# Performance work log

Hardware: AMD Instinct MI355X
Metric: run time of the kernel (lower is better)

Reference implementation:

```python
import jax, jax.numpy as jnp
import numpy as np

S = 4096      # total packed tokens
B = 8         # number of variable-length segments
E = 1152      # embed_dim (SigLIP2 so400m)
H = 16        # num_heads
D = E // H    # head_dim = 72


def setup_inputs() -> dict:
    key = jax.random.key(0)
    ks = jax.random.split(key, 8)
    w_std = 0.02
    theta = jax.random.uniform(ks[1], (S, D), jnp.float32, 0.0, 2.0 * np.pi)
    return {
        "hidden_states": jax.random.normal(ks[0], (S, E), jnp.float32),
        "cu_seqlens": jnp.arange(B + 1, dtype=jnp.int32) * (S // B),
        "cos": jnp.cos(theta),
        "sin": jnp.sin(theta),
        "Wq": jax.random.normal(ks[2], (E, E), jnp.float32) * w_std,
        "bq": jnp.zeros((E,), jnp.float32),
        "Wk": jax.random.normal(ks[3], (E, E), jnp.float32) * w_std,
        "bk": jnp.zeros((E,), jnp.float32),
        "Wv": jax.random.normal(ks[4], (E, E), jnp.float32) * w_std,
        "bv": jnp.zeros((E,), jnp.float32),
        "Wo": jax.random.normal(ks[5], (E, E), jnp.float32) * w_std,
        "bo": jnp.zeros((E,), jnp.float32),
    }


def _rotate_half(x):
    x1, x2 = jnp.split(x, 2, axis=-1)
    return jnp.concatenate((-x2, x1), axis=-1)


def reference(hidden_states, cu_seqlens, cos, sin, Wq, bq, Wk, bk, Wv, bv, Wo, bo):
    seq_len = hidden_states.shape[0]
    scale = np.float32(D) ** -0.5
    # projections -> [S, H, D]
    q = (hidden_states @ Wq.T + bq).reshape(seq_len, H, D)
    k = (hidden_states @ Wk.T + bk).reshape(seq_len, H, D)
    v = (hidden_states @ Wv.T + bv).reshape(seq_len, H, D)
    # inline RoPE (apply_rotary_pos_emb_vision): cos/sin broadcast over heads
    c = cos[:, None, :]
    s = sin[:, None, :]
    q = q * c + _rotate_half(q) * s
    k = k * c + _rotate_half(k) * s
    # segment id per token from cu_seqlens; block-diagonal attention mask
    seg = jnp.searchsorted(cu_seqlens[1:], jnp.arange(seq_len, dtype=cu_seqlens.dtype), side="right")
    mask = seg[:, None] == seg[None, :]                     # [S, S]
    scores = jnp.einsum("shd,thd->hst", q, k) * scale       # [H, S, S]
    neg = jnp.finfo(scores.dtype).min
    scores = jnp.where(mask[None, :, :], scores, neg)
    probs = jax.nn.softmax(scores, axis=-1)
    attn = jnp.einsum("hst,thd->shd", probs, v).reshape(seq_len, E)
    return attn @ Wo.T + bo
```

## Files before the change

kernel.cpp:

```cpp
#include <hip/hip_runtime.h>
#include <float.h>

#define S_LEN 4096
#define E_DIM 1152
#define NH    16
#define HD    72
#define HD2   36
#define NQKV  3456

typedef __attribute__((ext_vector_type(4))) float f32x4;
typedef __attribute__((ext_vector_type(8))) _Float16 f16x8;

__device__ __forceinline__ unsigned short f2h(float f) {
    union { _Float16 h; unsigned short u; } c;
    c.h = (_Float16)f;
    return c.u;
}

__device__ __forceinline__ void gload_lds16(const unsigned short* g, unsigned short* l) {
    __builtin_amdgcn_global_load_lds(
        (const __attribute__((address_space(1))) unsigned int*)g,
        (__attribute__((address_space(3))) unsigned int*)l, 16, 0, 0);
}

__global__ __launch_bounds__(256)
void pack_f16(const float* __restrict__ hs, const float* __restrict__ wq,
              const float* __restrict__ wk, const float* __restrict__ wv,
              const float* __restrict__ wo,
              unsigned short* __restrict__ hs_h, unsigned short* __restrict__ wqkv_h,
              unsigned short* __restrict__ wo_h)
{
    const float* src; unsigned short* dst; int n4;
    const int WSZ = E_DIM * E_DIM;
    switch (blockIdx.z) {
        case 0: src = hs; dst = hs_h;             n4 = S_LEN * E_DIM / 4; break;
        case 1: src = wq; dst = wqkv_h;           n4 = WSZ / 4; break;
        case 2: src = wk; dst = wqkv_h + WSZ;     n4 = WSZ / 4; break;
        case 3: src = wv; dst = wqkv_h + 2 * WSZ; n4 = WSZ / 4; break;
        default: src = wo; dst = wo_h;            n4 = WSZ / 4; break;
    }
    for (int i = blockIdx.x * 256 + threadIdx.x; i < n4; i += gridDim.x * 256) {
        f32x4 x = ((const f32x4*)src)[i];
        ushort4 hv;
        hv.x = f2h(x[0]); hv.y = f2h(x[1]); hv.z = f2h(x[2]); hv.w = f2h(x[3]);
        ((ushort4*)dst)[i] = hv;
    }
}

__global__ __launch_bounds__(256, 4)
void gemm_qkv_f16(const unsigned short* __restrict__ Ah, const unsigned short* __restrict__ Wh,
                  const float* __restrict__ bq, const float* __restrict__ bk,
                  const float* __restrict__ bv,
                  float* __restrict__ oq, float* __restrict__ ok,
                  unsigned short* __restrict__ vt)
{
    __shared__ unsigned short sA[128 * 64];
    __shared__ unsigned short sB[128 * 64];
    const int tid  = threadIdx.x;
    const int w    = tid >> 6, lane = tid & 63;
    const int quad = lane >> 4, m = lane & 15;
    const int wr   = w & 1,  wc = w >> 1;

    const int bid = blockIdx.x;
    const int lin = (bid & 7) * 108 + (bid >> 3);
    const int n_t = lin >> 5;
    const int m_t = lin & 31;
    const int m0  = m_t * 128;
    const int n0  = n_t * 128;

    const int srow = lane >> 3;
    const int skc  = (lane & 7) ^ srow;

    f32x4 acc[4][4];
    #pragma unroll
    for (int i = 0; i < 4; ++i)
        #pragma unroll
        for (int j = 0; j < 4; ++j) acc[i][j] = (f32x4){0.f, 0.f, 0.f, 0.f};

    const int rm7 = m & 7;

    for (int k0 = 0; k0 < E_DIM; k0 += 64) {
        #pragma unroll
        for (int c = 0; c < 4; ++c) {
            int r = 32 * w + 8 * c + srow;
            gload_lds16(Ah + (size_t)(m0 + r) * E_DIM + k0 + skc * 8, &sA[(32 * w + 8 * c) * 64]);
            gload_lds16(Wh + (size_t)(n0 + r) * E_DIM + k0 + skc * 8, &sB[(32 * w + 8 * c) * 64]);
        }
        __syncthreads();

        #pragma unroll
        for (int k3 = 0; k3 < 2; ++k3) {
            f16x8 ah[4], bh[4];
            #pragma unroll
            for (int t = 0; t < 4; ++t) {
                int pc = ((k3 << 2) + quad) ^ rm7;
                ah[t] = *(const f16x8*)&sA[(64 * wr + 16 * t + m) * 64 + pc * 8];
                bh[t] = *(const f16x8*)&sB[(64 * wc + 16 * t + m) * 64 + pc * 8];
            }
            #pragma unroll
            for (int rt = 0; rt < 4; ++rt)
                #pragma unroll
                for (int ct = 0; ct < 4; ++ct)
                    acc[rt][ct] = __builtin_amdgcn_mfma_f32_16x16x32_f16(ah[rt], bh[ct], acc[rt][ct], 0, 0, 0);
        }
        __syncthreads();
    }

    const int which = n0 / E_DIM;
    const int n0l = n0 - which * E_DIM;
    if (which < 2) {
        const float* bp = (which == 0) ? bq : bk;
        float* Cp       = (which == 0) ? oq : ok;
        #pragma unroll
        for (int ct = 0; ct < 4; ++ct) {
            int col = n0l + 64 * wc + 16 * ct + m;
            float bias = bp[col];
            #pragma unroll
            for (int rt = 0; rt < 4; ++rt)
                #pragma unroll
                for (int reg = 0; reg < 4; ++reg) {
                    int row = m0 + 64 * wr + 16 * rt + 4 * quad + reg;
                    Cp[(size_t)row * E_DIM + col] = acc[rt][ct][reg] + bias;
                }
        }
    } else {
        #pragma unroll
        for (int ct = 0; ct < 4; ++ct) {
            int vcol = n0l + 64 * wc + 16 * ct + m;
            int hh = vcol / HD, dd = vcol - hh * HD;
            float bias = bv[vcol];
            unsigned short* vrow = vt + ((size_t)hh * HD + dd) * S_LEN;
            #pragma unroll
            for (int rt = 0; rt < 4; ++rt) {
                int s0r = m0 + 64 * wr + 16 * rt + 4 * quad;
                ushort4 o;
                o.x = f2h(acc[rt][ct][0] + bias);
                o.y = f2h(acc[rt][ct][1] + bias);
                o.z = f2h(acc[rt][ct][2] + bias);
                o.w = f2h(acc[rt][ct][3] + bias);
                *(ushort4*)&vrow[s0r] = o;
            }
        }
    }
}

__global__ __launch_bounds__(256, 4)
void gemm_out_f16(const unsigned short* __restrict__ Ah, const unsigned short* __restrict__ Wh,
                  const float* __restrict__ bo, float* __restrict__ Cp)
{
    __shared__ unsigned short sA[64 * 64];
    __shared__ unsigned short sB[128 * 64];
    const int tid  = threadIdx.x;
    const int w    = tid >> 6, lane = tid & 63;
    const int quad = lane >> 4, m = lane & 15;
    const int m0   = blockIdx.y * 64;
    const int n0   = blockIdx.x * 128;

    const int srow = lane >> 3;
    const int skc  = (lane & 7) ^ srow;

    f32x4 acc[4][2];
    #pragma unroll
    for (int i = 0; i < 4; ++i)
        #pragma unroll
        for (int j = 0; j < 2; ++j) acc[i][j] = (f32x4){0.f, 0.f, 0.f, 0.f};

    const int rm7 = m & 7;

    for (int k0 = 0; k0 < E_DIM; k0 += 64) {
        #pragma unroll
        for (int c = 0; c < 2; ++c) {
            int r = 16 * w + 8 * c + srow;
            gload_lds16(Ah + (size_t)(m0 + r) * E_DIM + k0 + skc * 8, &sA[(16 * w + 8 * c) * 64]);
        }
        #pragma unroll
        for (int c = 0; c < 4; ++c) {
            int r = 32 * w + 8 * c + srow;
            gload_lds16(Wh + (size_t)(n0 + r) * E_DIM + k0 + skc * 8, &sB[(32 * w + 8 * c) * 64]);
        }
        __syncthreads();
        #pragma unroll
        for (int k3 = 0; k3 < 2; ++k3) {
            f16x8 ah[4], bh[2];
            int pc = ((k3 << 2) + quad) ^ rm7;
            #pragma unroll
            for (int t = 0; t < 4; ++t)
                ah[t] = *(const f16x8*)&sA[(16 * t + m) * 64 + pc * 8];
            #pragma unroll
            for (int ct = 0; ct < 2; ++ct)
                bh[ct] = *(const f16x8*)&sB[(32 * w + 16 * ct + m) * 64 + pc * 8];
            #pragma unroll
            for (int rt = 0; rt < 4; ++rt)
                #pragma unroll
                for (int ct = 0; ct < 2; ++ct)
                    acc[rt][ct] = __builtin_amdgcn_mfma_f32_16x16x32_f16(ah[rt], bh[ct], acc[rt][ct], 0, 0, 0);
        }
        __syncthreads();
    }

    #pragma unroll
    for (int ct = 0; ct < 2; ++ct) {
        int col = n0 + 32 * w + 16 * ct + m;
        float bias = bo[col];
        #pragma unroll
        for (int rt = 0; rt < 4; ++rt)
            #pragma unroll
            for (int reg = 0; reg < 4; ++reg) {
                int row = m0 + 16 * rt + 4 * quad + reg;
                Cp[(size_t)row * E_DIM + col] = acc[rt][ct][reg] + bias;
            }
    }
}

__global__ __launch_bounds__(256)
void prep_k(const float* __restrict__ kf, const float* __restrict__ cosb,
            const float* __restrict__ sinb, unsigned short* __restrict__ kh)
{
    const int h  = blockIdx.y;
    const int s0 = blockIdx.x * 64;
    for (int task = threadIdx.x; task < 64 * 9; task += 256) {
        int row = task / 9, d0 = (task % 9) << 2;
        int s = s0 + row;
        const float* xr = kf + (size_t)s * E_DIM + h * HD;
        f32x4 a  = *(const f32x4*)(xr + d0);
        f32x4 b  = *(const f32x4*)(xr + d0 + HD2);
        f32x4 c1 = *(const f32x4*)(cosb + (size_t)s * HD + d0);
        f32x4 s1 = *(const f32x4*)(sinb + (size_t)s * HD + d0);
        f32x4 c2 = *(const f32x4*)(cosb + (size_t)s * HD + d0 + HD2);
        f32x4 s2 = *(const f32x4*)(sinb + (size_t)s * HD + d0 + HD2);
        f32x4 r1 = a * c1 - b * s1;
        f32x4 r2 = b * c2 + a * s2;
        uint2 u1, u2;
        u1.x = (unsigned)f2h(r1[0]) | ((unsigned)f2h(r1[1]) << 16);
        u1.y = (unsigned)f2h(r1[2]) | ((unsigned)f2h(r1[3]) << 16);
        u2.x = (unsigned)f2h(r2[0]) | ((unsigned)f2h(r2[1]) << 16);
        u2.y = (unsigned)f2h(r2[2]) | ((unsigned)f2h(r2[3]) << 16);
        unsigned short* orow = kh + ((size_t)h * S_LEN + s) * HD;
        *(uint2*)&orow[d0]       = u1;
        *(uint2*)&orow[d0 + HD2] = u2;
    }
}

__global__ __launch_bounds__(256, 4)
void attn_f16(const float* __restrict__ qf, const float* __restrict__ cosb,
              const float* __restrict__ sinb, const unsigned short* __restrict__ kh,
              const unsigned short* __restrict__ vt, const int* __restrict__ cu,
              int nseg, unsigned short* __restrict__ out)
{
    __shared__ unsigned short ks_s[64][72];
    __shared__ unsigned short vs_s[80][72];
    __shared__ unsigned short ss_s[64][72];

    const int tid  = threadIdx.x;
    const int w    = tid >> 6;
    const int lane = tid & 63;
    const int quad = lane >> 4;
    const int m    = lane & 15;
    const int h    = blockIdx.y;
    const int qb0  = blockIdx.x * 64;
    const float cexp = 0.17002324f;

    {
        uint4 zz = make_uint4(0u, 0u, 0u, 0u);
        if (tid < 72) {
            int r = 72 + tid / 9, c = tid % 9;
            *(uint4*)&vs_s[r][c << 3] = zz;
        }
    }

    int rs_r[4], re_r[4];
    #pragma unroll
    for (int reg = 0; reg < 4; ++reg) {
        int row = qb0 + 16 * w + 4 * quad + reg;
        int st = 0;
        for (int i = 1; i < nseg; ++i) if (cu[i] <= row) st = i;
        rs_r[reg] = cu[st];
        re_r[reg] = cu[st + 1];
    }
    int st0 = 0, st1 = 0;
    for (int i = 1; i < nseg; ++i) {
        if (cu[i] <= qb0) st0 = i;
        if (cu[i] <= qb0 + 63) st1 = i;
    }
    const int kstart = cu[st0];
    const int kend   = cu[st1 + 1];
    const bool aligned = (st0 == st1);

    const unsigned short* ktbase = kh + (size_t)h * S_LEN * HD;
    const unsigned short* vtbase = vt + (size_t)h * HD * S_LEN;
    unsigned short* ksf = &ks_s[0][0];

    const int sl0 = tid, sl1 = tid + 256;
    const int sl2 = (tid < 64) ? tid + 512 : tid + 256;
    const int vd0 = sl0 >> 3, vc0 = (sl0 & 7) << 3;
    const int vd1 = sl1 >> 3, vc1 = (sl1 & 7) << 3;
    const int vd2 = sl2 >> 3, vc2 = (sl2 & 7) << 3;

    uint4 kp0, kp1, kp2, vp0, vp1, vp2;
    {
        const unsigned short* kt = ktbase + (size_t)kstart * HD;
        kp0 = *(const uint4*)(kt + sl0 * 8);
        kp1 = *(const uint4*)(kt + sl1 * 8);
        kp2 = *(const uint4*)(kt + sl2 * 8);
        vp0 = *(const uint4*)(vtbase + (size_t)vd0 * S_LEN + kstart + vc0);
        vp1 = *(const uint4*)(vtbase + (size_t)vd1 * S_LEN + kstart + vc1);
        vp2 = *(const uint4*)(vtbase + (size_t)vd2 * S_LEN + kstart + vc2);
    }

    for (int task = tid; task < 64 * 9; task += 256) {
        int row = task / 9, d0 = (task % 9) << 2;
        int s = qb0 + row;
        const float* xr = qf + (size_t)s * E_DIM + h * HD;
        f32x4 a  = *(const f32x4*)(xr + d0);
        f32x4 b  = *(const f32x4*)(xr + d0 + HD2);
        f32x4 c1 = *(const f32x4*)(cosb + (size_t)s * HD + d0);
        f32x4 s1 = *(const f32x4*)(sinb + (size_t)s * HD + d0);
        f32x4 c2 = *(const f32x4*)(cosb + (size_t)s * HD + d0 + HD2);
        f32x4 s2 = *(const f32x4*)(sinb + (size_t)s * HD + d0 + HD2);
        f32x4 r1 = a * c1 - b * s1;
        f32x4 r2 = b * c2 + a * s2;
        uint2 u1, u2;
        u1.x = (unsigned)f2h(r1[0]) | ((unsigned)f2h(r1[1]) << 16);
        u1.y = (unsigned)f2h(r1[2]) | ((unsigned)f2h(r1[3]) << 16);
        u2.x = (unsigned)f2h(r2[0]) | ((unsigned)f2h(r2[1]) << 16);
        u2.y = (unsigned)f2h(r2[2]) | ((unsigned)f2h(r2[3]) << 16);
        *(uint2*)&ks_s[row][d0]       = u1;
        *(uint2*)&ks_s[row][d0 + HD2] = u2;
    }
    __syncthreads();

    f16x8 qfr[3];
    {
        const unsigned short* qrow = &ks_s[16 * w + m][0];
        #pragma unroll
        for (int k3 = 0; k3 < 3; ++k3) {
            bool pad = (k3 == 2) && (quad != 0);
            int off = pad ? 0 : (k3 * 32 + quad * 8);
            f16x8 val = *(const f16x8*)(qrow + off);
            f16x8 z = {0, 0, 0, 0, 0, 0, 0, 0};
            qfr[k3] = pad ? z : val;
        }
    }

    f32x4 acc_o[5];
    #pragma unroll
    for (int i = 0; i < 5; ++i) acc_o[i] = (f32x4){0.f, 0.f, 0.f, 0.f};
    float l_r[4] = {0.f, 0.f, 0.f, 0.f};

    for (int kb = kstart; kb < kend; kb += 64) {
        __syncthreads();
        *(uint4*)(ksf + sl0 * 8) = kp0;
        *(uint4*)(ksf + sl1 * 8) = kp1;
        if (tid < 64) *(uint4*)(ksf + sl2 * 8) = kp2;
        *(uint4*)&vs_s[vd0][vc0] = vp0;
        *(uint4*)&vs_s[vd1][vc1] = vp1;
        if (tid < 64) *(uint4*)&vs_s[vd2][vc2] = vp2;
        __syncthreads();

        int kn = kb + 64;
        if (kn < kend) {
            const unsigned short* kt = ktbase + (size_t)kn * HD;
            kp0 = *(const uint4*)(kt + sl0 * 8);
            kp1 = *(const uint4*)(kt + sl1 * 8);
            kp2 = *(const uint4*)(kt + sl2 * 8);
            vp0 = *(const uint4*)(vtbase + (size_t)vd0 * S_LEN + kn + vc0);
            vp1 = *(const uint4*)(vtbase + (size_t)vd1 * S_LEN + kn + vc1);
            vp2 = *(const uint4*)(vtbase + (size_t)vd2 * S_LEN + kn + vc2);
        }

        f32x4 sacc[4];
        #pragma unroll
        for (int ct = 0; ct < 4; ++ct) sacc[ct] = (f32x4){0.f, 0.f, 0.f, 0.f};
        #pragma unroll
        for (int ct = 0; ct < 4; ++ct) {
            const unsigned short* krow = &ks_s[16 * ct + m][0];
            #pragma unroll
            for (int k3 = 0; k3 < 3; ++k3) {
                bool pad = (k3 == 2) && (quad != 0);
                int off = pad ? 0 : (k3 * 32 + quad * 8);
                f16x8 bfr = *(const f16x8*)(krow + off);
                f16x8 z = {0, 0, 0, 0, 0, 0, 0, 0};
                bfr = pad ? z : bfr;
                sacc[ct] = __builtin_amdgcn_mfma_f32_16x16x32_f16(qfr[k3], bfr, sacc[ct], 0, 0, 0);
            }
        }

        if (aligned) {
            #pragma unroll
            for (int ct = 0; ct < 4; ++ct)
                #pragma unroll
                for (int reg = 0; reg < 4; ++reg) {
                    float p = __builtin_amdgcn_exp2f(sacc[ct][reg] * cexp);
                    l_r[reg] += p;
                    ss_s[16 * w + 4 * quad + reg][16 * ct + m] = f2h(p);
                }
        } else {
            #pragma unroll
            for (int ct = 0; ct < 4; ++ct) {
                int key = kb + 16 * ct + m;
                #pragma unroll
                for (int reg = 0; reg < 4; ++reg) {
                    bool valid = (key >= rs_r[reg]) && (key < re_r[reg]);
                    float p = valid ? __builtin_amdgcn_exp2f(sacc[ct][reg] * cexp) : 0.f;
                    l_r[reg] += p;
                    ss_s[16 * w + 4 * quad + reg][16 * ct + m] = f2h(p);
                }
            }
        }

        {
            const unsigned short* prow = &ss_s[16 * w + m][0];
            f16x8 pf0 = *(const f16x8*)(prow + quad * 8);
            f16x8 pf1 = *(const f16x8*)(prow + 32 + quad * 8);
            #pragma unroll
            for (int ct2 = 0; ct2 < 5; ++ct2) {
                const unsigned short* vrow = &vs_s[16 * ct2 + m][0];
                f16x8 vf0 = *(const f16x8*)(vrow + quad * 8);
                f16x8 vf1 = *(const f16x8*)(vrow + 32 + quad * 8);
                acc_o[ct2] = __builtin_amdgcn_mfma_f32_16x16x32_f16(pf0, vf0, acc_o[ct2], 0, 0, 0);
                acc_o[ct2] = __builtin_amdgcn_mfma_f32_16x16x32_f16(pf1, vf1, acc_o[ct2], 0, 0, 0);
            }
        }
    }

    #pragma unroll
    for (int reg = 0; reg < 4; ++reg) {
        float l = l_r[reg];
        l += __shfl_xor(l, 1);
        l += __shfl_xor(l, 2);
        l += __shfl_xor(l, 4);
        l += __shfl_xor(l, 8);
        l_r[reg] = l;
    }

    #pragma unroll
    for (int reg = 0; reg < 4; ++reg) {
        float linv = (l_r[reg] > 0.f) ? 1.f / l_r[reg] : 0.f;
        int row = qb0 + 16 * w + 4 * quad + reg;
        unsigned short* orow = out + (size_t)row * E_DIM + h * HD;
        #pragma unroll
        for (int ct2 = 0; ct2 < 5; ++ct2) {
            int col = 16 * ct2 + m;
            float v  = acc_o[ct2][reg] * linv;
            float pv = __shfl_xor(v, 1);
            if (!(m & 1) && col < HD) {
                unsigned dw = (unsigned)f2h(v) | ((unsigned)f2h(pv) << 16);
                *(unsigned*)&orow[col] = dw;
            }
        }
    }
}

extern "C" void kernel_launch(void* const* d_in, const int* in_sizes, int n_in,
                              void* d_out, int out_size, void* d_ws, size_t ws_size,
                              hipStream_t stream)
{
    const float* hs   = (const float*)d_in[0];
    const int*   cu   = (const int*)d_in[1];
    const float* cosb = (const float*)d_in[2];
    const float* sinb = (const float*)d_in[3];
    const float* Wq   = (const float*)d_in[4];
    const float* bq   = (const float*)d_in[5];
    const float* Wk   = (const float*)d_in[6];
    const float* bk   = (const float*)d_in[7];
    const float* Wv   = (const float*)d_in[8];
    const float* bv   = (const float*)d_in[9];
    const float* Wo   = (const float*)d_in[10];
    const float* bo   = (const float*)d_in[11];
    float* outp = (float*)d_out;

    const size_t mat = (size_t)S_LEN * E_DIM;
    float* qf = (float*)d_ws;
    float* kf = qf + mat;
    unsigned short* hs_h   = (unsigned short*)(kf + mat);
    unsigned short* wqkv_h = hs_h + mat;
    unsigned short* wo_h   = wqkv_h + (size_t)NQKV * E_DIM;
    unsigned short* vtb    = wo_h + (size_t)E_DIM * E_DIM;
    unsigned short* kh     = hs_h;
    unsigned short* attn_h = (unsigned short*)kf;

    const int nseg = in_sizes[1] - 1;

    dim3 gpack(512, 1, 5);
    pack_f16<<<gpack, 256, 0, stream>>>(hs, Wq, Wk, Wv, Wo, hs_h, wqkv_h, wo_h);

    gemm_qkv_f16<<<dim3(864), 256, 0, stream>>>(hs_h, wqkv_h, bq, bk, bv, qf, kf, vtb);

    dim3 gprep(S_LEN / 64, NH, 1);
    prep_k<<<gprep, 256, 0, stream>>>(kf, cosb, sinb, kh);

    dim3 gattn(S_LEN / 64, NH, 1);
    attn_f16<<<gattn, 256, 0, stream>>>(qf, cosb, sinb, kh, vtb, cu, nseg, attn_h);

    dim3 gout(E_DIM / 128, S_LEN / 64, 1);
    gemm_out_f16<<<gout, 256, 0, stream>>>(attn_h, wo_h, bo, outp);
}
```

Before: 207.1 us.

## Rewrite QKV GEMM with 256x128 tiles and triple-buffered async LDS pipeline

Replaces the 128x128 single-buffered QKV projection GEMM with a 512-thread, 256x128-tile kernel that triple-buffers A/B tiles in LDS. Global-to-LDS loads for the stage two k-steps ahead are interleaved with the MFMA phases, using explicit vmcnt waits, barriers and s_setprio. The aim is to hide load latency and cut per-k-step sync stalls. In exchange it uses about 144KB of LDS per block, which limits occupancy, and the grid shrinks to 432 blocks, which may hurt wave balance.

```diff
diff --git a/kernel.cpp b/kernel.cpp
--- a/kernel.cpp
+++ b/kernel.cpp
@@ -7,6 +7,7 @@
 #define HD    72
 #define HD2   36
 #define NQKV  3456
+#define NTK   18
 
 typedef __attribute__((ext_vector_type(4))) float f32x4;
 typedef __attribute__((ext_vector_type(8))) _Float16 f16x8;
@@ -47,29 +48,30 @@
     }
 }
 
-__global__ __launch_bounds__(256, 4)
-void gemm_qkv_f16(const unsigned short* __restrict__ Ah, const unsigned short* __restrict__ Wh,
-                  const float* __restrict__ bq, const float* __restrict__ bk,
-                  const float* __restrict__ bv,
-                  float* __restrict__ oq, float* __restrict__ ok,
-                  unsigned short* __restrict__ vt)
+__global__ __launch_bounds__(512, 2)
+void gemm_qkv_dp(const unsigned short* __restrict__ Ah, const unsigned short* __restrict__ Wh,
+                 const float* __restrict__ bq, const float* __restrict__ bk,
+                 const float* __restrict__ bv,
+                 float* __restrict__ oq, float* __restrict__ ok,
+                 unsigned short* __restrict__ vt)
 {
-    __shared__ unsigned short sA[128 * 64];
-    __shared__ unsigned short sB[128 * 64];
+    __shared__ unsigned short sA[3][256 * 64];
+    __shared__ unsigned short sB[3][128 * 64];
     const int tid  = threadIdx.x;
     const int w    = tid >> 6, lane = tid & 63;
     const int quad = lane >> 4, m = lane & 15;
-    const int wr   = w & 1,  wc = w >> 1;
+    const int wm   = w >> 1, wn = w & 1;
 
     const int bid = blockIdx.x;
-    const int lin = (bid & 7) * 108 + (bid >> 3);
-    const int n_t = lin >> 5;
-    const int m_t = lin & 31;
-    const int m0  = m_t * 128;
+    const int lin = (bid & 7) * 54 + (bid >> 3);
+    const int m_t = lin & 15;
+    const int n_t = lin >> 4;
+    const int m0  = m_t * 256;
     const int n0  = n_t * 128;
 
     const int srow = lane >> 3;
     const int skc  = (lane & 7) ^ srow;
+    const int rm7  = m & 7;
 
     f32x4 acc[4][4];
     #pragma unroll
@@ -77,33 +79,87 @@
         #pragma unroll
         for (int j = 0; j < 4; ++j) acc[i][j] = (f32x4){0.f, 0.f, 0.f, 0.f};
 
-    const int rm7 = m & 7;
-
-    for (int k0 = 0; k0 < E_DIM; k0 += 64) {
-        #pragma unroll
-        for (int c = 0; c < 4; ++c) {
-            int r = 32 * w + 8 * c + srow;
-            gload_lds16(Ah + (size_t)(m0 + r) * E_DIM + k0 + skc * 8, &sA[(32 * w + 8 * c) * 64]);
-            gload_lds16(Wh + (size_t)(n0 + r) * E_DIM + k0 + skc * 8, &sB[(32 * w + 8 * c) * 64]);
-        }
-        __syncthreads();
-
-        #pragma unroll
-        for (int k3 = 0; k3 < 2; ++k3) {
-            f16x8 ah[4], bh[4];
-            #pragma unroll
-            for (int t = 0; t < 4; ++t) {
+    auto stageA = [&](int buf, int k0, int gi) {
+        int r0 = (w + gi * 8) * 8;
+        gload_lds16(Ah + (size_t)(m0 + r0 + srow) * E_DIM + k0 + skc * 8, &sA[buf][r0 * 64]);
+    };
+    auto stageB = [&](int buf, int k0, int gi) {
+        int r0 = (w + gi * 8) * 8;
+        gload_lds16(Wh + (size_t)(n0 + r0 + srow) * E_DIM + k0 + skc * 8, &sB[buf][r0 * 64]);
+    };
+
+    #pragma unroll
+    for (int gi = 0; gi < 4; ++gi) stageA(0, 0, gi);
+    #pragma unroll
+    for (int gi = 0; gi < 2; ++gi) stageB(0, 0, gi);
+    #pragma unroll
+    for (int gi = 0; gi < 4; ++gi) stageA(1, 64, gi);
+    #pragma unroll
+    for (int gi = 0; gi < 2; ++gi) stageB(1, 64, gi);
+    asm volatile("s_waitcnt vmcnt(6)" ::: "memory");
+    __builtin_amdgcn_s_barrier();
+    __builtin_amdgcn_sched_barrier(0);
+
+    for (int g = 0; g < NTK; ++g) {
+        const int b  = g % 3;
+        const int sb = (g + 2) % 3;
+        const int ks = (g + 2) * 64;
+        const bool st = (g + 2) < NTK;
+        const unsigned short* pA = &sA[b][0];
+        const unsigned short* pB = &sB[b][0];
+
+        f16x8 ah[4][2], bh[2][2];
+        #pragma unroll
+        for (int rt = 0; rt < 4; ++rt)
+            #pragma unroll
+            for (int k3 = 0; k3 < 2; ++k3) {
                 int pc = ((k3 << 2) + quad) ^ rm7;
-                ah[t] = *(const f16x8*)&sA[(64 * wr + 16 * t + m) * 64 + pc * 8];
-                bh[t] = *(const f16x8*)&sB[(64 * wc + 16 * t + m) * 64 + pc * 8];
-            }
-            #pragma unroll
-            for (int rt = 0; rt < 4; ++rt)
+                ah[rt][k3] = *(const f16x8*)&pA[(wm * 64 + 16 * rt + m) * 64 + pc * 8];
+            }
+        #pragma unroll
+        for (int ct = 0; ct < 2; ++ct)
+            #pragma unroll
+            for (int k3 = 0; k3 < 2; ++k3) {
+                int pc = ((k3 << 2) + quad) ^ rm7;
+                bh[ct][k3] = *(const f16x8*)&pB[(wn * 64 + 16 * ct + m) * 64 + pc * 8];
+            }
+        if (st) { stageA(sb, ks, 0); stageA(sb, ks, 1); stageB(sb, ks, 0); }
+        __builtin_amdgcn_s_barrier();
+        __builtin_amdgcn_sched_barrier(0);
+        __builtin_amdgcn_s_setprio(1);
+        #pragma unroll
+        for (int rt = 0; rt < 4; ++rt)
+            #pragma unroll
+            for (int ct = 0; ct < 2; ++ct)
                 #pragma unroll
-                for (int ct = 0; ct < 4; ++ct)
-                    acc[rt][ct] = __builtin_amdgcn_mfma_f32_16x16x32_f16(ah[rt], bh[ct], acc[rt][ct], 0, 0, 0);
-        }
-        __syncthreads();
+                for (int k3 = 0; k3 < 2; ++k3)
+                    acc[rt][ct] = __builtin_amdgcn_mfma_f32_16x16x32_f16(ah[rt][k3], bh[ct][k3], acc[rt][ct], 0, 0, 0);
+        __builtin_amdgcn_s_setprio(0);
+        __builtin_amdgcn_s_barrier();
+        __builtin_amdgcn_sched_barrier(0);
+        #pragma unroll
+        for (int ct = 0; ct < 2; ++ct)
+            #pragma unroll
+            for (int k3 = 0; k3 < 2; ++k3) {
+                int pc = ((k3 << 2) + quad) ^ rm7;
+                bh[ct][k3] = *(const f16x8*)&pB[(wn * 64 + 16 * (ct + 2) + m) * 64 + pc * 8];
+            }
+        if (st) { stageA(sb, ks, 2); stageA(sb, ks, 3); stageB(sb, ks, 1); }
+        __builtin_amdgcn_s_barrier();
+        __builtin_amdgcn_sched_barrier(0);
+        __builtin_amdgcn_s_setprio(1);
+        #pragma unroll
+        for (int rt = 0; rt < 4; ++rt)
+            #pragma unroll
+            for (int ct = 0; ct < 2; ++ct)
+                #pragma unroll
+                for (int k3 = 0; k3 < 2; ++k3)
+                    acc[rt][ct + 2] = __builtin_amdgcn_mfma_f32_16x16x32_f16(ah[rt][k3], bh[ct][k3], acc[rt][ct + 2], 0, 0, 0);
+        __builtin_amdgcn_s_setprio(0);
+        if (st) asm volatile("s_waitcnt vmcnt(6)" ::: "memory");
+        else    asm volatile("s_waitcnt vmcnt(0)" ::: "memory");
+        __builtin_amdgcn_s_barrier();
+        __builtin_amdgcn_sched_barrier(0);
     }
 
     const int which = n0 / E_DIM;
@@ -113,26 +169,26 @@
         float* Cp       = (which == 0) ? oq : ok;
         #pragma unroll
         for (int ct = 0; ct < 4; ++ct) {
-            int col = n0l + 64 * wc + 16 * ct + m;
+            int col = n0l + wn * 64 + 16 * ct + m;
             float bias = bp[col];
             #pragma unroll
             for (int rt = 0; rt < 4; ++rt)
                 #pragma unroll
                 for (int reg = 0; reg < 4; ++reg) {
-                    int row = m0 + 64 * wr + 16 * rt + 4 * quad + reg;
+                    int row = m0 + wm * 64 + 16 * rt + 4 * quad + reg;
                     Cp[(size_t)row * E_DIM + col] = acc[rt][ct][reg] + bias;
                 }
         }
     } else {
         #pragma unroll
         for (int ct = 0; ct < 4; ++ct) {
-            int vcol = n0l + 64 * wc + 16 * ct + m;
+            int vcol = n0l + wn * 64 + 16 * ct + m;
             int hh = vcol / HD, dd = vcol - hh * HD;
             float bias = bv[vcol];
             unsigned short* vrow = vt + ((size_t)hh * HD + dd) * S_LEN;
             #pragma unroll
             for (int rt = 0; rt < 4; ++rt) {
-                int s0r = m0 + 64 * wr + 16 * rt + 4 * quad;
+                int s0r = m0 + wm * 64 + 16 * rt + 4 * quad;
                 ushort4 o;
                 o.x = f2h(acc[rt][ct][0] + bias);
                 o.y = f2h(acc[rt][ct][1] + bias);
@@ -484,7 +540,7 @@
     dim3 gpack(512, 1, 5);
     pack_f16<<<gpack, 256, 0, stream>>>(hs, Wq, Wk, Wv, Wo, hs_h, wqkv_h, wo_h);
 
-    gemm_qkv_f16<<<dim3(864), 256, 0, stream>>>(hs_h, wqkv_h, bq, bk, bv, qf, kf, vtb);
+    gemm_qkv_dp<<<dim3(432), 512, 0, stream>>>(hs_h, wqkv_h, bq, bk, bv, qf, kf, vtb);
 
     dim3 gprep(S_LEN / 64, NH, 1);
     prep_k<<<gprep, 256, 0, stream>>>(kf, cosb, sinb, kh);
```

Measured after the change: 213.0 us. 2.9% more time.
